# Performance work log

Hardware: AMD Instinct MI355X
Metric: run time of the kernel (lower is better)

## Reference

```python
import jax, jax.numpy as jnp
import numpy as np

N_NODES = 10000
N_EDGES = 160000
D_IN = 50
ALPHA = 0.2  # LeakyReLU negative slope


def _xavier(key, shape):
    fan_in, fan_out = shape[0], int(np.prod(shape[1:]))
    limit = float(np.sqrt(6.0 / (fan_in + fan_out)))
    return jax.random.uniform(key, shape, jnp.float32, -limit, limit)


def setup_inputs() -> dict:
    key = jax.random.key(0)
    ks = jax.random.split(key, 8)
    x = jax.random.normal(ks[0], (N_NODES, D_IN), jnp.float32)
    edge_idx = jax.random.randint(ks[1], (2, N_EDGES), 0, N_NODES, jnp.int64)
    # layer 1: 50 -> 4 heads x 256, concat
    W1 = _xavier(ks[2], (D_IN, 4, 256))
    a1 = _xavier(ks[3], (4, 512))  # [H, 2F]: split into a_src, a_dst
    # layer 2: 1024 -> 4 heads x 256, concat
    W2 = _xavier(ks[4], (1024, 4, 256))
    a2 = _xavier(ks[5], (4, 512))
    # layer 3: 1024 -> 6 heads x 121, mean
    W3 = _xavier(ks[6], (1024, 6, 121))
    a3 = _xavier(ks[7], (6, 242))
    return {"x": x, "edge_idx": edge_idx, "W1": W1, "a1": a1,
            "W2": W2, "a2": a2, "W3": W3, "a3": a3}


def gat_layer(h, W, a, src, dst, aggregate):
    """Multi-head GAT layer over an edge list. h:[N,Din], W:[Din,H,F], a:[H,2F]."""
    N = h.shape[0]
    Wh = jnp.einsum('nd,dhf->nhf', h, W)                    # [N, H, F]
    F = Wh.shape[-1]
    att_src = jnp.einsum('nhf,hf->nh', Wh, a[:, :F])         # a^T [Wh_i || .]
    att_dst = jnp.einsum('nhf,hf->nh', Wh, a[:, F:])         # a^T [. || Wh_j]
    logits = jax.nn.leaky_relu(att_src[src] + att_dst[dst], ALPHA)  # [E, H]
    # numerically stable softmax over incoming edges of each destination node
    m = jax.ops.segment_max(logits, dst, num_segments=N)
    e = jnp.exp(logits - m[dst])
    denom = jax.ops.segment_sum(e, dst, num_segments=N)
    coef = e / (denom[dst] + 1e-16)                           # [E, H]
    out = jax.ops.segment_sum(coef[:, :, None] * Wh[src], dst, num_segments=N)
    if aggregate == 'concat':
        return out.reshape(N, -1)
    return out.mean(axis=1)


def reference(x, edge_idx, W1, a1, W2, a2, W3, a3):
    src, dst = edge_idx[0], edge_idx[1]
    h1 = jax.nn.elu(gat_layer(x, W1, a1, src, dst, 'concat'))   # [N, 1024]
    h2 = jax.nn.elu(gat_layer(h1, W2, a2, src, dst, 'concat'))  # [N, 1024]
    h3_in = h1 + h2                                              # residual skip
    return gat_layer(h3_in, W3, a3, src, dst, 'mean')            # [N, 121]
```

## Files before the change

### kernel.cpp

```cpp
#include <hip/hip_runtime.h>
#include <hip/hip_bf16.h>
#include <math.h>

#define NN 10000
#define NE 160000

typedef __attribute__((ext_vector_type(8))) _Float16 f16x8;
typedef __attribute__((ext_vector_type(4))) _Float16 f16x4;
typedef __attribute__((ext_vector_type(4))) float f32x4;

static __device__ __forceinline__ void gload_lds16(const _Float16* g, _Float16* l) {
  __builtin_amdgcn_global_load_lds((const __attribute__((address_space(1))) char*)g,
                                   (__attribute__((address_space(3))) char*)l, 16, 0, 0);
}

__global__ __launch_bounds__(1024) void scan_kernel(const int* __restrict__ counts,
                                                    int* __restrict__ row_ptr,
                                                    int* __restrict__ cursor, int N) {
  __shared__ int sums[1024];
  int t = threadIdx.x;
  const int CH = (N + 1023) >> 10;
  int base = t * CH;
  int s = 0;
  for (int i = 0; i < CH; ++i) { int idx = base + i; if (idx < N) s += counts[idx]; }
  sums[t] = s;
  __syncthreads();
  for (int off = 1; off < 1024; off <<= 1) {
    int v = 0;
    if (t >= off) v = sums[t - off];
    __syncthreads();
    if (t >= off) sums[t] += v;
    __syncthreads();
  }
  int run = (t == 0) ? 0 : sums[t - 1];
  for (int i = 0; i < CH; ++i) {
    int idx = base + i;
    if (idx < N) { row_ptr[idx] = run; cursor[idx] = run; run += counts[idx]; }
  }
  if (t == 0) row_ptr[N] = sums[1023];
}

__global__ void scatter_kernel(const int* __restrict__ src, const int* __restrict__ dst,
                               int* __restrict__ cursor, int* __restrict__ ssrc, int E) {
  int e = blockIdx.x * blockDim.x + threadIdx.x;
  if (e < E) {
    int pos = atomicAdd(&cursor[dst[e]], 1);
    ssrc[pos] = src[e];
  }
}

#define TB_W2 256
#define TB_W3 192
#define TB_W1 16
#define TB_T (TB_W2 + TB_W3 + TB_W1)
#define TB_X ((NN * 64) / 256)
#define TB_E ((NE + 255) / 256)
__global__ __launch_bounds__(256) void prep2(const float* __restrict__ x,
                                             const float* __restrict__ W1,
                                             const float* __restrict__ W2,
                                             const float* __restrict__ W3,
                                             const int* __restrict__ dst,
                                             int* __restrict__ counts,
                                             _Float16* __restrict__ xh,
                                             _Float16* __restrict__ w1,
                                             _Float16* __restrict__ w2,
                                             _Float16* __restrict__ w3) {
  int b = blockIdx.x;
  int t = threadIdx.x;
  if (b < TB_T) {
    const float* S;
    _Float16* D;
    int K, Nsrc, KP, k0, n0;
    if (b < TB_W2) {
      S = W2; D = w2; K = 1024; Nsrc = 1024; KP = 1024;
      k0 = (b & 15) * 64; n0 = (b >> 4) * 64;
    } else if (b < TB_W2 + TB_W3) {
      int bb = b - TB_W2;
      S = W3; D = w3; K = 1024; Nsrc = 726; KP = 1024;
      k0 = (bb & 15) * 64; n0 = (bb >> 4) * 64;
    } else {
      int bb = b - TB_W2 - TB_W3;
      S = W1; D = w1; K = 50; Nsrc = 1024; KP = 64;
      k0 = 0; n0 = bb * 64;
    }
    __shared__ float tile[64][65];
#pragma unroll
    for (int i = 0; i < 16; ++i) {
      int idx = i * 256 + t;
      int r = idx >> 6, c = idx & 63;
      int gk = k0 + r, gn = n0 + c;
      tile[r][c] = (gk < K && gn < Nsrc) ? S[(size_t)gk * Nsrc + gn] : 0.f;
    }
    __syncthreads();
#pragma unroll
    for (int i = 0; i < 16; ++i) {
      int idx = i * 256 + t;
      int r = idx >> 6, c = idx & 63;
      D[(size_t)(n0 + r) * KP + k0 + c] = (_Float16)tile[c][r];
    }
    return;
  }
  int i = (b - TB_T) * 256 + t;
  if (i < NN * 64) {
    int m = i >> 6, k = i & 63;
    xh[i] = (_Float16)(k < 50 ? x[m * 50 + k] : 0.f);
    return;
  }
  i -= NN * 64;
  if (i < NE) atomicAdd(&counts[dst[i]], 1);
}

template<int PAD121>
__global__ __launch_bounds__(256) void gemm_f16(const _Float16* __restrict__ A,
                                                const _Float16* __restrict__ B,
                                                _Float16* __restrict__ C,
                                                int M, int KP, int NC) {
  int flat = blockIdx.x;
  int xcd = flat & 7;
  int slot = flat >> 3;
  int cblk = slot % NC;
  int rblk = (slot / NC) * 8 + xcd;
  const int m0 = rblk * 128;
  if (m0 >= M) return;
  const int n0 = cblk * 128;

  __shared__ _Float16 As[128 * 64];
  __shared__ _Float16 Bs[128 * 64];

  const int t = threadIdx.x;
  const int lane = t & 63;
  const int wid = t >> 6;
  const int wr = wid >> 1;
  const int wc = wid & 1;
  const int row_in = lane & 15;
  const int kgrp = lane >> 4;

  const int srow = wid * 32 + ((lane >> 3) & 7);
  const int sl7 = lane & 7;

  f32x4 acc[4][4];
#pragma unroll
  for (int i = 0; i < 4; ++i)
#pragma unroll
    for (int j = 0; j < 4; ++j) acc[i][j] = (f32x4){0.f, 0.f, 0.f, 0.f};

  for (int k0 = 0; k0 < KP; k0 += 64) {
    if (k0) __syncthreads();
#pragma unroll
    for (int j = 0; j < 4; ++j) {
      int row = srow + j * 8;
      int gs = (sl7 ^ (row & 7)) * 8;
      int gm = m0 + row;
      if (gm >= M) gm = M - 1;
      _Float16* ldsA = &As[(wid * 32 + j * 8) * 64];
      _Float16* ldsB = &Bs[(wid * 32 + j * 8) * 64];
      gload_lds16(&A[(size_t)gm * KP + k0 + gs], ldsA);
      gload_lds16(&B[(size_t)(n0 + row) * KP + k0 + gs], ldsB);
    }
    __syncthreads();

#pragma unroll
    for (int ks = 0; ks < 2; ++ks) {
      f16x8 a[4], b[4];
#pragma unroll
      for (int mi = 0; mi < 4; ++mi) {
        int arow = wr * 64 + mi * 16 + row_in;
        int ps = ((kgrp + ks * 4) ^ (arow & 7)) * 8;
        a[mi] = *(const f16x8*)&As[arow * 64 + ps];
      }
#pragma unroll
      for (int ni = 0; ni < 4; ++ni) {
        int brow = wc * 64 + ni * 16 + row_in;
        int ps = ((kgrp + ks * 4) ^ (brow & 7)) * 8;
        b[ni] = *(const f16x8*)&Bs[brow * 64 + ps];
      }
#pragma unroll
      for (int mi = 0; mi < 4; ++mi)
#pragma unroll
        for (int ni = 0; ni < 4; ++ni)
          acc[mi][ni] = __builtin_amdgcn_mfma_f32_16x16x32_f16(a[mi], b[ni], acc[mi][ni], 0, 0, 0);
    }
  }

#pragma unroll
  for (int mi = 0; mi < 4; ++mi) {
#pragma unroll
    for (int ni = 0; ni < 4; ++ni) {
      int gn = n0 + wc * 64 + ni * 16 + row_in;
#pragma unroll
      for (int j = 0; j < 4; ++j) {
        int gm = m0 + wr * 64 + mi * 16 + kgrp * 4 + j;
        if (gm >= M) continue;
        if (PAD121) {
          if (gn < 726) {
            int h = gn / 121;
            int pc = h * 128 + (gn - h * 121);
            C[(size_t)gm * 768 + pc] = (_Float16)acc[mi][ni][j];
          }
        } else {
          C[(size_t)gm * 1024 + gn] = (_Float16)acc[mi][ni][j];
        }
      }
    }
  }
}

template<int H, int F, int SW, int HS>
__global__ void att_kernel(const _Float16* __restrict__ Whb, const float* __restrict__ a,
                           float* __restrict__ att_s, float* __restrict__ att_d, int N) {
  int n = blockIdx.x;
  int h = threadIdx.x >> 6;
  int lane = threadIdx.x & 63;
  const _Float16* w = Whb + (size_t)n * SW + h * HS;
  const float* as = a + (size_t)h * 2 * F;
  const float* ad = as + F;
  float ss = 0.f, sd = 0.f;
  if (F == 256) {
    f16x4 wv = *(const f16x4*)&w[lane * 4];
    f32x4 av = *(const f32x4*)&as[lane * 4];
    f32x4 dv = *(const f32x4*)&ad[lane * 4];
#pragma unroll
    for (int j = 0; j < 4; ++j) {
      float v = (float)wv[j];
      ss += v * av[j];
      sd += v * dv[j];
    }
  } else {
    for (int f = lane; f < F; f += 64) {
      float v = (float)w[f];
      ss += v * as[f];
      sd += v * ad[f];
    }
  }
#pragma unroll
  for (int off = 32; off > 0; off >>= 1) {
    ss += __shfl_down(ss, off);
    sd += __shfl_down(sd, off);
  }
  if (lane == 0) {
    att_s[n * H + h] = ss;
    att_d[n * H + h] = sd;
  }
}

template<int H>
__global__ __launch_bounds__(256) void edge_softmax_csr(const int* __restrict__ row_ptr,
                                                        const int* __restrict__ ssrc,
                                                        const float* __restrict__ att_s,
                                                        const float* __restrict__ att_d,
                                                        float* __restrict__ cbuf,
                                                        float* __restrict__ dinv, int N) {
  int n = blockIdx.x * 16 + (threadIdx.x >> 4);
  if (n >= N) return;
  int lane = threadIdx.x & 15;
  int beg = row_ptr[n], end = row_ptr[n + 1];

  float ad[H];
  if (H == 4) {
    f32x4 v = *(const f32x4*)&att_d[n * 4];
    ad[0] = v.x; ad[1] = v.y; ad[2] = v.z; ad[3] = v.w;
  } else {
#pragma unroll
    for (int h = 0; h < H; ++h) ad[h] = att_d[n * H + h];
  }

  float m[H];
#pragma unroll
  for (int h = 0; h < H; ++h) m[h] = -1e30f;
  for (int k = beg + lane; k < end; k += 16) {
    int s = ssrc[k];
    float as[H];
    if (H == 4) {
      f32x4 v = *(const f32x4*)&att_s[s * 4];
      as[0] = v.x; as[1] = v.y; as[2] = v.z; as[3] = v.w;
    } else {
#pragma unroll
      for (int h = 0; h < H; ++h) as[h] = att_s[s * H + h];
    }
#pragma unroll
    for (int h = 0; h < H; ++h) {
      float xv = as[h] + ad[h];
      float l = xv >= 0.f ? xv : 0.2f * xv;
      m[h] = fmaxf(m[h], l);
    }
  }
#pragma unroll
  for (int h = 0; h < H; ++h)
#pragma unroll
    for (int off = 8; off > 0; off >>= 1) m[h] = fmaxf(m[h], __shfl_xor(m[h], off));

  float sum[H];
#pragma unroll
  for (int h = 0; h < H; ++h) sum[h] = 0.f;
  for (int k = beg + lane; k < end; k += 16) {
    int s = ssrc[k];
    float as[H];
    if (H == 4) {
      f32x4 v = *(const f32x4*)&att_s[s * 4];
      as[0] = v.x; as[1] = v.y; as[2] = v.z; as[3] = v.w;
    } else {
#pragma unroll
      for (int h = 0; h < H; ++h) as[h] = att_s[s * H + h];
    }
    float ev[H];
#pragma unroll
    for (int h = 0; h < H; ++h) {
      float xv = as[h] + ad[h];
      float l = xv >= 0.f ? xv : 0.2f * xv;
      ev[h] = __expf(l - m[h]);
      sum[h] += ev[h];
    }
    if (H == 4) {
      *(f32x4*)&cbuf[(size_t)k * 4] = (f32x4){ev[0], ev[1], ev[2], ev[3]};
    } else {
#pragma unroll
      for (int h = 0; h < H; ++h) cbuf[(size_t)k * H + h] = ev[h];
    }
  }
#pragma unroll
  for (int h = 0; h < H; ++h) {
#pragma unroll
    for (int off = 8; off > 0; off >>= 1) sum[h] += __shfl_xor(sum[h], off);
  }
  if (lane < H) dinv[n * H + lane] = 1.f / (sum[lane] + 1e-16f);
}

template<int MODE>
__global__ __launch_bounds__(256) void aggregate_cat_chunk(const int* __restrict__ row_ptr,
                                                           const int* __restrict__ ssrc,
                                                           const float* __restrict__ cbuf,
                                                           const float* __restrict__ dinv,
                                                           const _Float16* __restrict__ Whb,
                                                           const _Float16* __restrict__ h1,
                                                           _Float16* __restrict__ outv, int N) {
  int b = blockIdx.x;
  int chunk = b & 7;
  int group = b >> 3;
  int n = group * 8 + (threadIdx.x >> 5);
  if (n >= N) return;
  int l32 = threadIdx.x & 31;
  int half = l32 >> 4;
  int tt = l32 & 15;
  int idx = chunk * 128 + tt * 8;
  int h = chunk >> 1;
  float inv = dinv[n * 4 + h];

  float acc[8] = {};
  int beg = row_ptr[n], end = row_ptr[n + 1];
  int k = beg + half;
  for (; k + 6 < end; k += 8) {
    int s0 = ssrc[k], s1 = ssrc[k + 2], s2 = ssrc[k + 4], s3 = ssrc[k + 6];
    float c0 = cbuf[(size_t)k * 4 + h];
    float c1 = cbuf[(size_t)(k + 2) * 4 + h];
    float c2 = cbuf[(size_t)(k + 4) * 4 + h];
    float c3 = cbuf[(size_t)(k + 6) * 4 + h];
    f16x8 w0 = *(const f16x8*)&Whb[(size_t)s0 * 1024 + idx];
    f16x8 w1 = *(const f16x8*)&Whb[(size_t)s1 * 1024 + idx];
    f16x8 w2 = *(const f16x8*)&Whb[(size_t)s2 * 1024 + idx];
    f16x8 w3 = *(const f16x8*)&Whb[(size_t)s3 * 1024 + idx];
#pragma unroll
    for (int j = 0; j < 8; ++j) {
      acc[j] += c0 * (float)w0[j];
      acc[j] += c1 * (float)w1[j];
      acc[j] += c2 * (float)w2[j];
      acc[j] += c3 * (float)w3[j];
    }
  }
  for (; k < end; k += 2) {
    int s0 = ssrc[k];
    float c0 = cbuf[(size_t)k * 4 + h];
    f16x8 w0 = *(const f16x8*)&Whb[(size_t)s0 * 1024 + idx];
#pragma unroll
    for (int j = 0; j < 8; ++j) acc[j] += c0 * (float)w0[j];
  }
#pragma unroll
  for (int j = 0; j < 8; ++j) acc[j] += __shfl_xor(acc[j], 16);

  if (half == 0) {
    size_t o = (size_t)n * 1024 + idx;
    f16x8 r1;
    if (MODE == 1) r1 = *(const f16x8*)&h1[o];
    f16x8 vo;
#pragma unroll
    for (int j = 0; j < 8; ++j) {
      float v = acc[j] * inv;
      v = v > 0.f ? v : expm1f(v);
      if (MODE == 1) v += (float)r1[j];
      vo[j] = (_Float16)v;
    }
    *(f16x8*)&outv[o] = vo;
  }
}

__global__ __launch_bounds__(256) void aggregate_mean_chunk(const int* __restrict__ row_ptr,
                                                            const int* __restrict__ ssrc,
                                                            const float* __restrict__ cbuf,
                                                            const float* __restrict__ dinv,
                                                            const _Float16* __restrict__ Whb,
                                                            float* __restrict__ part, int N) {
  int b = blockIdx.x;
  int h = b & 7;
  if (h >= 6) return;
  int n = (b >> 3) * 8 + (threadIdx.x >> 5);
  if (n >= N) return;
  int l32 = threadIdx.x & 31;
  int half = l32 >> 4;
  int tt = l32 & 15;
  int base = h * 128 + tt * 8;
  float inv = dinv[n * 6 + h];

  float acc[8] = {};
  int beg = row_ptr[n], end = row_ptr[n + 1];
  int k = beg + half;
  for (; k + 6 < end; k += 8) {
    int s0 = ssrc[k], s1 = ssrc[k + 2], s2 = ssrc[k + 4], s3 = ssrc[k + 6];
    float c0 = cbuf[(size_t)k * 6 + h];
    float c1 = cbuf[(size_t)(k + 2) * 6 + h];
    float c2 = cbuf[(size_t)(k + 4) * 6 + h];
    float c3 = cbuf[(size_t)(k + 6) * 6 + h];
    f16x8 w0 = *(const f16x8*)&Whb[(size_t)s0 * 768 + base];
    f16x8 w1 = *(const f16x8*)&Whb[(size_t)s1 * 768 + base];
    f16x8 w2 = *(const f16x8*)&Whb[(size_t)s2 * 768 + base];
    f16x8 w3 = *(const f16x8*)&Whb[(size_t)s3 * 768 + base];
#pragma unroll
    for (int j = 0; j < 8; ++j) {
      acc[j] += c0 * (float)w0[j];
      acc[j] += c1 * (float)w1[j];
      acc[j] += c2 * (float)w2[j];
      acc[j] += c3 * (float)w3[j];
    }
  }
  for (; k < end; k += 2) {
    int s0 = ssrc[k];
    float c0 = cbuf[(size_t)k * 6 + h];
    f16x8 w0 = *(const f16x8*)&Whb[(size_t)s0 * 768 + base];
#pragma unroll
    for (int j = 0; j < 8; ++j) acc[j] += c0 * (float)w0[j];
  }
#pragma unroll
  for (int j = 0; j < 8; ++j) acc[j] += __shfl_xor(acc[j], 16);

  if (half == 0) {
    float* p = &part[(size_t)n * 768 + base];
    *(f32x4*)&p[0] = (f32x4){acc[0] * inv, acc[1] * inv, acc[2] * inv, acc[3] * inv};
    *(f32x4*)&p[4] = (f32x4){acc[4] * inv, acc[5] * inv, acc[6] * inv, acc[7] * inv};
  }
}

__global__ __launch_bounds__(128) void reduce_mean(const float* __restrict__ part,
                                                   float* __restrict__ out, int N) {
  int n = blockIdx.x;
  int f = threadIdx.x;
  if (f >= 121) return;
  const float* p = &part[(size_t)n * 768];
  float s = 0.f;
#pragma unroll
  for (int h = 0; h < 6; ++h) s += p[h * 128 + f];
  out[(size_t)n * 121 + f] = s * (1.0f / 6.0f);
}

extern "C" void kernel_launch(void* const* d_in, const int* in_sizes, int n_in,
                              void* d_out, int out_size, void* d_ws, size_t ws_size,
                              hipStream_t stream) {
  const float* x  = (const float*)d_in[0];
  const int* eidx = (const int*)d_in[1];
  const float* W1 = (const float*)d_in[2];
  const float* a1 = (const float*)d_in[3];
  const float* W2 = (const float*)d_in[4];
  const float* a2 = (const float*)d_in[5];
  const float* W3 = (const float*)d_in[6];
  const float* a3 = (const float*)d_in[7];
  float* out = (float*)d_out;

  const int N = NN, E = NE;
  const int* src = eidx;
  const int* dst = eidx + E;

  char* ws = (char*)d_ws;
  size_t off = 0;
  auto alloc = [&](size_t bytes) -> void* {
    void* p = ws + off;
    off += (bytes + 255) & ~(size_t)255;
    return p;
  };
  _Float16* Whf  = (_Float16*)alloc((size_t)N * 1024 * 2);
  _Float16* h1   = (_Float16*)alloc((size_t)N * 1024 * 2);
  _Float16* hsum = (_Float16*)alloc((size_t)N * 1024 * 2);
  _Float16* xh   = (_Float16*)alloc((size_t)N * 64 * 2);
  _Float16* w1   = (_Float16*)alloc((size_t)1024 * 64 * 2);
  _Float16* w2   = (_Float16*)alloc((size_t)1024 * 1024 * 2);
  _Float16* w3   = (_Float16*)alloc((size_t)768 * 1024 * 2);
  float* cbuf  = (float*)alloc((size_t)E * 6 * 4);
  float* part  = (float*)alloc((size_t)N * 768 * 4);
  float* atts  = (float*)alloc((size_t)N * 6 * 4);
  float* attd  = (float*)alloc((size_t)N * 6 * 4);
  float* dinv  = (float*)alloc((size_t)N * 6 * 4);
  int* counts  = (int*)alloc((size_t)N * 4);
  int* row_ptr = (int*)alloc((size_t)(N + 1) * 4);
  int* cursor  = (int*)alloc((size_t)N * 4);
  int* ssrc    = (int*)alloc((size_t)E * 4);

  hipMemsetAsync(counts, 0, (size_t)N * 4, stream);
  prep2<<<TB_T + TB_X + TB_E, 256, 0, stream>>>(x, W1, W2, W3, dst, counts, xh, w1, w2, w3);
  scan_kernel<<<1, 1024, 0, stream>>>(counts, row_ptr, cursor, N);
  scatter_kernel<<<(E + 255) / 256, 256, 0, stream>>>(src, dst, cursor, ssrc, E);

  const int RPG = 10;
  const int AGG_GRID = 8 * ((N + 7) / 8);
  const int SM_GRID = (N + 15) / 16;

  gemm_f16<0><<<8 * RPG * 8, 256, 0, stream>>>(xh, w1, Whf, N, 64, 8);
  att_kernel<4, 256, 1024, 256><<<N, 256, 0, stream>>>(Whf, a1, atts, attd, N);
  edge_softmax_csr<4><<<SM_GRID, 256, 0, stream>>>(row_ptr, ssrc, atts, attd, cbuf, dinv, N);
  aggregate_cat_chunk<0><<<AGG_GRID, 256, 0, stream>>>(row_ptr, ssrc, cbuf, dinv, Whf, nullptr, h1, N);

  gemm_f16<0><<<8 * RPG * 8, 256, 0, stream>>>(h1, w2, Whf, N, 1024, 8);
  att_kernel<4, 256, 1024, 256><<<N, 256, 0, stream>>>(Whf, a2, atts, attd, N);
  edge_softmax_csr<4><<<SM_GRID, 256, 0, stream>>>(row_ptr, ssrc, atts, attd, cbuf, dinv, N);
  aggregate_cat_chunk<1><<<AGG_GRID, 256, 0, stream>>>(row_ptr, ssrc, cbuf, dinv, Whf, h1, hsum, N);

  gemm_f16<1><<<8 * RPG * 6, 256, 0, stream>>>(hsum, w3, Whf, N, 1024, 6);
  att_kernel<6, 121, 768, 128><<<N, 384, 0, stream>>>(Whf, a3, atts, attd, N);
  edge_softmax_csr<6><<<SM_GRID, 256, 0, stream>>>(row_ptr, ssrc, atts, attd, cbuf, dinv, N);
  aggregate_mean_chunk<<<AGG_GRID, 256, 0, stream>>>(row_ptr, ssrc, cbuf, dinv, Whf, part, N);
  reduce_mean<<<N, 128, 0, stream>>>(part, out, N);
}
```

Baseline: 263.6 us.

## Fold attention vectors into weights and compute scores inside the GEMM

Precomputes W·a_src and W·a_dst per head as small fp16 matrices in the prep kernel, then has column-block-0 blocks of each GEMM compute the attention logits with extra MFMAs on the already-loaded A fragments. This removes the three separate att_kernel launches and their re-read of the fp16 Wh output. In exchange the attention projections now come from fp16-rounded folded weights rather than from Wh, which changes rounding, and the extra work in cblk 0 blocks reads the folded-weight operand directly from global memory and creates load imbalance across blocks.

```diff
diff --git a/kernel.cpp b/kernel.cpp
--- a/kernel.cpp
+++ b/kernel.cpp
@@ -55,16 +55,26 @@
 #define TB_T (TB_W2 + TB_W3 + TB_W1)
 #define TB_X ((NN * 64) / 256)
 #define TB_E ((NE + 255) / 256)
+#define WT1 (16 * 64)
+#define WT2 (16 * 1024)
+#define WT3 (16 * 1024)
+#define TB_WT ((WT1 + WT2 + WT3) / 256)
 __global__ __launch_bounds__(256) void prep2(const float* __restrict__ x,
                                              const float* __restrict__ W1,
+                                             const float* __restrict__ a1,
                                              const float* __restrict__ W2,
+                                             const float* __restrict__ a2,
                                              const float* __restrict__ W3,
+                                             const float* __restrict__ a3,
                                              const int* __restrict__ dst,
                                              int* __restrict__ counts,
                                              _Float16* __restrict__ xh,
                                              _Float16* __restrict__ w1,
                                              _Float16* __restrict__ w2,
-                                             _Float16* __restrict__ w3) {
+                                             _Float16* __restrict__ w3,
+                                             _Float16* __restrict__ wt1,
+                                             _Float16* __restrict__ wt2,
+                                             _Float16* __restrict__ wt3) {
   int b = blockIdx.x;
   int t = threadIdx.x;
   if (b < TB_T) {
@@ -107,14 +117,72 @@
     return;
   }
   i -= NN * 64;
-  if (i < NE) atomicAdd(&counts[dst[i]], 1);
+  if (i < NE) { atomicAdd(&counts[dst[i]], 1); return; }
+  i -= NE;
+  if (i < WT1) {
+    int j = i >> 6, k = i & 63;
+    float v = 0.f;
+    if (j < 8 && k < 50) {
+      int h = j & 3, side = j >> 2;
+      const float* wp = W1 + k * 1024 + h * 256;
+      const float* ap = a1 + h * 512 + side * 256;
+      float s = 0.f;
+      for (int f = 0; f < 256; f += 4) {
+        f32x4 wv = *(const f32x4*)&wp[f];
+        f32x4 av = *(const f32x4*)&ap[f];
+        s += wv.x * av.x + wv.y * av.y + wv.z * av.z + wv.w * av.w;
+      }
+      v = s;
+    }
+    wt1[i] = (_Float16)v;
+    return;
+  }
+  i -= WT1;
+  if (i < WT2) {
+    int j = i >> 10, k = i & 1023;
+    float v = 0.f;
+    if (j < 8) {
+      int h = j & 3, side = j >> 2;
+      const float* wp = W2 + k * 1024 + h * 256;
+      const float* ap = a2 + h * 512 + side * 256;
+      float s = 0.f;
+      for (int f = 0; f < 256; f += 4) {
+        f32x4 wv = *(const f32x4*)&wp[f];
+        f32x4 av = *(const f32x4*)&ap[f];
+        s += wv.x * av.x + wv.y * av.y + wv.z * av.z + wv.w * av.w;
+      }
+      v = s;
+    }
+    wt2[i] = (_Float16)v;
+    return;
+  }
+  i -= WT2;
+  if (i < WT3) {
+    int j = i >> 10, k = i & 1023;
+    float v = 0.f;
+    if (j < 12) {
+      int h = (j < 6) ? j : j - 6;
+      int side = (j < 6) ? 0 : 1;
+      const float* wp = W3 + k * 726 + h * 121;
+      const float* ap = a3 + h * 242 + side * 121;
+      float s = 0.f;
+#pragma unroll 11
+      for (int f = 0; f < 121; ++f) s += wp[f] * ap[f];
+      v = s;
+    }
+    wt3[i] = (_Float16)v;
+    return;
+  }
 }
 
 template<int PAD121>
 __global__ __launch_bounds__(256) void gemm_f16(const _Float16* __restrict__ A,
                                                 const _Float16* __restrict__ B,
+                                                const _Float16* __restrict__ wtilT,
                                                 _Float16* __restrict__ C,
-                                                int M, int KP, int NC) {
+                                                float* __restrict__ atts,
+                                                float* __restrict__ attd,
+                                                int M, int KP, int NC, int hh) {
   int flat = blockIdx.x;
   int xcd = flat & 7;
   int slot = flat >> 3;
@@ -137,12 +205,16 @@
 
   const int srow = wid * 32 + ((lane >> 3) & 7);
   const int sl7 = lane & 7;
+  const bool do_att = (cblk == 0) && (wc == 0);
 
   f32x4 acc[4][4];
 #pragma unroll
   for (int i = 0; i < 4; ++i)
 #pragma unroll
     for (int j = 0; j < 4; ++j) acc[i][j] = (f32x4){0.f, 0.f, 0.f, 0.f};
+  f32x4 acc_att[4];
+#pragma unroll
+  for (int i = 0; i < 4; ++i) acc_att[i] = (f32x4){0.f, 0.f, 0.f, 0.f};
 
   for (int k0 = 0; k0 < KP; k0 += 64) {
     if (k0) __syncthreads();
@@ -179,6 +251,12 @@
 #pragma unroll
         for (int ni = 0; ni < 4; ++ni)
           acc[mi][ni] = __builtin_amdgcn_mfma_f32_16x16x32_f16(a[mi], b[ni], acc[mi][ni], 0, 0, 0);
+      if (do_att) {
+        f16x8 bt = *(const f16x8*)&wtilT[(size_t)row_in * KP + k0 + ks * 32 + kgrp * 8];
+#pragma unroll
+        for (int mi = 0; mi < 4; ++mi)
+          acc_att[mi] = __builtin_amdgcn_mfma_f32_16x16x32_f16(a[mi], bt, acc_att[mi], 0, 0, 0);
+      }
     }
   }
 
@@ -203,43 +281,19 @@
       }
     }
   }
-}
-
-template<int H, int F, int SW, int HS>
-__global__ void att_kernel(const _Float16* __restrict__ Whb, const float* __restrict__ a,
-                           float* __restrict__ att_s, float* __restrict__ att_d, int N) {
-  int n = blockIdx.x;
-  int h = threadIdx.x >> 6;
-  int lane = threadIdx.x & 63;
-  const _Float16* w = Whb + (size_t)n * SW + h * HS;
-  const float* as = a + (size_t)h * 2 * F;
-  const float* ad = as + F;
-  float ss = 0.f, sd = 0.f;
-  if (F == 256) {
-    f16x4 wv = *(const f16x4*)&w[lane * 4];
-    f32x4 av = *(const f32x4*)&as[lane * 4];
-    f32x4 dv = *(const f32x4*)&ad[lane * 4];
-#pragma unroll
-    for (int j = 0; j < 4; ++j) {
-      float v = (float)wv[j];
-      ss += v * av[j];
-      sd += v * dv[j];
-    }
-  } else {
-    for (int f = lane; f < F; f += 64) {
-      float v = (float)w[f];
-      ss += v * as[f];
-      sd += v * ad[f];
-    }
-  }
-#pragma unroll
-  for (int off = 32; off > 0; off >>= 1) {
-    ss += __shfl_down(ss, off);
-    sd += __shfl_down(sd, off);
-  }
-  if (lane == 0) {
-    att_s[n * H + h] = ss;
-    att_d[n * H + h] = sd;
+  if (do_att) {
+    int col = row_in;
+#pragma unroll
+    for (int mi = 0; mi < 4; ++mi) {
+#pragma unroll
+      for (int j = 0; j < 4; ++j) {
+        int gm = m0 + wr * 64 + mi * 16 + kgrp * 4 + j;
+        if (gm >= M) continue;
+        float v = acc_att[mi][j];
+        if (col < hh) atts[(size_t)gm * hh + col] = v;
+        else if (col < 2 * hh) attd[(size_t)gm * hh + col - hh] = v;
+      }
+    }
   }
 }
 
@@ -490,6 +544,9 @@
   _Float16* w1   = (_Float16*)alloc((size_t)1024 * 64 * 2);
   _Float16* w2   = (_Float16*)alloc((size_t)1024 * 1024 * 2);
   _Float16* w3   = (_Float16*)alloc((size_t)768 * 1024 * 2);
+  _Float16* wt1  = (_Float16*)alloc((size_t)16 * 64 * 2);
+  _Float16* wt2  = (_Float16*)alloc((size_t)16 * 1024 * 2);
+  _Float16* wt3  = (_Float16*)alloc((size_t)16 * 1024 * 2);
   float* cbuf  = (float*)alloc((size_t)E * 6 * 4);
   float* part  = (float*)alloc((size_t)N * 768 * 4);
   float* atts  = (float*)alloc((size_t)N * 6 * 4);
@@ -501,7 +558,9 @@
   int* ssrc    = (int*)alloc((size_t)E * 4);
 
   hipMemsetAsync(counts, 0, (size_t)N * 4, stream);
-  prep2<<<TB_T + TB_X + TB_E, 256, 0, stream>>>(x, W1, W2, W3, dst, counts, xh, w1, w2, w3);
+  prep2<<<TB_T + TB_X + TB_E + TB_WT, 256, 0, stream>>>(x, W1, a1, W2, a2, W3, a3,
+                                                        dst, counts, xh, w1, w2, w3,
+                                                        wt1, wt2, wt3);
   scan_kernel<<<1, 1024, 0, stream>>>(counts, row_ptr, cursor, N);
   scatter_kernel<<<(E + 255) / 256, 256, 0, stream>>>(src, dst, cursor, ssrc, E);
 
@@ -509,18 +568,15 @@
   const int AGG_GRID = 8 * ((N + 7) / 8);
   const int SM_GRID = (N + 15) / 16;
 
-  gemm_f16<0><<<8 * RPG * 8, 256, 0, stream>>>(xh, w1, Whf, N, 64, 8);
-  att_kernel<4, 256, 1024, 256><<<N, 256, 0, stream>>>(Whf, a1, atts, attd, N);
+  gemm_f16<0><<<8 * RPG * 8, 256, 0, stream>>>(xh, w1, wt1, Whf, atts, attd, N, 64, 8, 4);
   edge_softmax_csr<4><<<SM_GRID, 256, 0, stream>>>(row_ptr, ssrc, atts, attd, cbuf, dinv, N);
   aggregate_cat_chunk<0><<<AGG_GRID, 256, 0, stream>>>(row_ptr, ssrc, cbuf, dinv, Whf, nullptr, h1, N);
 
-  gemm_f16<0><<<8 * RPG * 8, 256, 0, stream>>>(h1, w2, Whf, N, 1024, 8);
-  att_kernel<4, 256, 1024, 256><<<N, 256, 0, stream>>>(Whf, a2, atts, attd, N);
+  gemm_f16<0><<<8 * RPG * 8, 256, 0, stream>>>(h1, w2, wt2, Whf, atts, attd, N, 1024, 8, 4);
   edge_softmax_csr<4><<<SM_GRID, 256, 0, stream>>>(row_ptr, ssrc, atts, attd, cbuf, dinv, N);
   aggregate_cat_chunk<1><<<AGG_GRID, 256, 0, stream>>>(row_ptr, ssrc, cbuf, dinv, Whf, h1, hsum, N);
 
-  gemm_f16<1><<<8 * RPG * 6, 256, 0, stream>>>(hsum, w3, Whf, N, 1024, 6);
-  att_kernel<6, 121, 768, 128><<<N, 384, 0, stream>>>(Whf, a3, atts, attd, N);
+  gemm_f16<1><<<8 * RPG * 6, 256, 0, stream>>>(hsum, w3, wt3, Whf, atts, attd, N, 1024, 6, 6);
   edge_softmax_csr<6><<<SM_GRID, 256, 0, stream>>>(row_ptr, ssrc, atts, attd, cbuf, dinv, N);
   aggregate_mean_chunk<<<AGG_GRID, 256, 0, stream>>>(row_ptr, ssrc, cbuf, dinv, Whf, part, N);
   reduce_mean<<<N, 128, 0, stream>>>(part, out, N);
```

New measurement: 263.2 us. Within noise of the previous version (-0.1%).
